# Kernel optimization log

Measured on AMD Instinct MI355X. Metric: run time of the kernel, lower is better.

## Reference

```python
import jax, jax.numpy as jnp
import numpy as np

M, D, K = 65536, 64, 4096
BETA = 0.25
INIT_STD = 0.1


def setup_inputs() -> dict:
    key = jax.random.key(0)
    k1, k2, k3 = jax.random.split(key, 3)
    z_e = jax.random.normal(k1, (M, D), dtype=jnp.float32)
    codebook_weight = jax.random.normal(k2, (K, D), dtype=jnp.float32) * INIT_STD
    ema_cluster_size = jax.random.uniform(k3, (K,), dtype=jnp.float32)
    return {"z_e": z_e, "codebook_weight": codebook_weight,
            "ema_cluster_size": ema_cluster_size}


def reference(z_e, codebook_weight, ema_cluster_size):
    # Squared-distance matrix: ||z||^2 + ||e||^2 - 2 z.e   -> (M, K)
    z2 = jnp.sum(z_e * z_e, axis=1, keepdims=True)            # (M, 1)
    e2 = jnp.sum(codebook_weight * codebook_weight, axis=1)[None, :]  # (1, K)
    ze = z_e @ codebook_weight.T                               # (M, K)
    dist = z2 + e2 - 2.0 * ze
    indices = jnp.argmin(dist, axis=1)                         # (M,)
    z_q = codebook_weight[indices]                             # (M, D)

    # use_ema=True path (eval mode: no EMA buffer update)
    commit_loss = jnp.mean((z_e - jax.lax.stop_gradient(z_q)) ** 2)
    vq_loss = BETA * commit_loss

    # Straight-through estimator
    z_q_st = z_e + jax.lax.stop_gradient(z_q - z_e)

    # Perplexity from EMA cluster-size buffer
    probs = ema_cluster_size + 1e-10
    probs = probs / jnp.sum(probs)
    perplexity = jnp.exp(-jnp.sum(probs * jnp.log(probs)))
    perplexity = jax.lax.stop_gradient(perplexity)

    return z_q_st, indices, vq_loss, perplexity, z_q
```

## Files before the change

kernel.cpp:

```cpp
#include <hip/hip_runtime.h>
#include <cmath>

#define M_ROWS  65536
#define D_DIM   64
#define K_CODES 4096

#define OFF_IDX  4194304
#define OFF_SCAL 4259840
#define OFF_ZQ   4259842

#define IMG_OFF   (4u << 20)
#define CANDB_OFF 17039368u

#define CH_BYTES 16384
#define CH_QUADS 1024
#define NSPLIT   4
#define NCHB     8

typedef _Float16 f16x8 __attribute__((ext_vector_type(8)));
typedef __attribute__((ext_vector_type(4))) float f32x4;
typedef unsigned long long u64;

__device__ __forceinline__ unsigned short f2h(float f) {
  _Float16 h = (_Float16)f;
  return __builtin_bit_cast(unsigned short, h);
}
__device__ __forceinline__ float h2f(unsigned short u) {
  return (float)__builtin_bit_cast(_Float16, u);
}
__device__ __forceinline__ unsigned int umin_(unsigned int a, unsigned int b) {
  return a < b ? a : b;
}
__device__ __forceinline__ unsigned int med3_u32(unsigned int a, unsigned int b, unsigned int c) {
  unsigned int d;
  asm("v_med3_u32 %0, %1, %2, %3" : "=v"(d) : "v"(a), "v"(b), "v"(c));
  return d;
}

__device__ __forceinline__ void gload_lds16(const void* g, void* l) {
  __builtin_amdgcn_global_load_lds((const __attribute__((address_space(1))) void*)g,
                                   (__attribute__((address_space(3))) void*)l, 16, 0, 0);
}
__device__ __forceinline__ void gload_lds4(const void* g, void* l) {
  __builtin_amdgcn_global_load_lds((const __attribute__((address_space(1))) void*)g,
                                   (__attribute__((address_space(3))) void*)l, 4, 0, 0);
}

__device__ __forceinline__ float exact_dist(const float4* z4, float z2,
                                            const float* __restrict__ cb,
                                            const float* __restrict__ e2, int k) {
  const float4* ev = (const float4*)(cb + (size_t)k * 64);
  float4 a0 = make_float4(0.f, 0.f, 0.f, 0.f);
  float4 a1 = make_float4(0.f, 0.f, 0.f, 0.f);
  float4 a2 = make_float4(0.f, 0.f, 0.f, 0.f);
  float4 a3 = make_float4(0.f, 0.f, 0.f, 0.f);
#pragma unroll
  for (int q = 0; q < 4; ++q) {
    float4 e0 = ev[4 * q + 0], e1 = ev[4 * q + 1], e2v = ev[4 * q + 2], e3 = ev[4 * q + 3];
    a0.x = fmaf(z4[4 * q + 0].x, e0.x, a0.x); a0.y = fmaf(z4[4 * q + 0].y, e0.y, a0.y);
    a0.z = fmaf(z4[4 * q + 0].z, e0.z, a0.z); a0.w = fmaf(z4[4 * q + 0].w, e0.w, a0.w);
    a1.x = fmaf(z4[4 * q + 1].x, e1.x, a1.x); a1.y = fmaf(z4[4 * q + 1].y, e1.y, a1.y);
    a1.z = fmaf(z4[4 * q + 1].z, e1.z, a1.z); a1.w = fmaf(z4[4 * q + 1].w, e1.w, a1.w);
    a2.x = fmaf(z4[4 * q + 2].x, e2v.x, a2.x); a2.y = fmaf(z4[4 * q + 2].y, e2v.y, a2.y);
    a2.z = fmaf(z4[4 * q + 2].z, e2v.z, a2.z); a2.w = fmaf(z4[4 * q + 2].w, e2v.w, a2.w);
    a3.x = fmaf(z4[4 * q + 3].x, e3.x, a3.x); a3.y = fmaf(z4[4 * q + 3].y, e3.y, a3.y);
    a3.z = fmaf(z4[4 * q + 3].z, e3.z, a3.z); a3.w = fmaf(z4[4 * q + 3].w, e3.w, a3.w);
  }
  float d;
  {
#pragma clang fp contract(off)
    float sx = (a0.x + a1.x) + (a2.x + a3.x);
    float sy = (a0.y + a1.y) + (a2.y + a3.y);
    float sz = (a0.z + a1.z) + (a2.z + a3.z);
    float sw = (a0.w + a1.w) + (a2.w + a3.w);
    float dot = (sx + sy) + (sz + sw);
    float tt = z2 + e2[k];
    d = tt - 2.0f * dot;
  }
  return d;
}

__device__ __forceinline__ float exact_z2(const float4* z4) {
#pragma clang fp contract(off)
  float rr[8];
  {
    const float* f = (const float*)&z4[0];
#pragma unroll
    for (int j = 0; j < 8; ++j) rr[j] = f[j] * f[j];
  }
#pragma unroll
  for (int a = 1; a < 8; ++a) {
    const float* f = (const float*)&z4[2 * a];
#pragma unroll
    for (int j = 0; j < 8; ++j) rr[j] = rr[j] + f[j] * f[j];
  }
  return ((rr[0] + rr[1]) + (rr[2] + rr[3])) + ((rr[4] + rr[5]) + (rr[6] + rr[7]));
}

__device__ __forceinline__ unsigned int ford(float f) {
  unsigned int b = __float_as_uint(f);
  return b ^ ((((int)b) >> 31) | 0x80000000u);
}

__global__ void prep_kernel(const float* __restrict__ cb, char* __restrict__ img,
                            float* __restrict__ e2, float* __restrict__ e2b) {
  int t = blockIdx.x * 256 + threadIdx.x;
  {
    int k  = t >> 4;
    int d0 = (t & 15) * 4;
    float4 f = ((const float4*)cb)[t];
    ushort4 hi;
    hi.x = f2h(f.x);
    hi.y = f2h(f.y);
    hi.z = f2h(f.z);
    hi.w = f2h(f.w);
    int c = k >> 7, r = k & 127;
    int g = d0 >> 3;
    int off = ((g + r) & 7) * 16 + (d0 & 7) * 2;
    char* base = img + (size_t)c * CH_BYTES + r * 128;
    *(ushort4*)(base + off) = hi;
  }
  if (t < K_CODES) {
    const float4* row = (const float4*)(cb + (size_t)t * D_DIM);
    float4 q[16];
#pragma unroll
    for (int i = 0; i < 16; ++i) q[i] = row[i];
    float s = exact_z2(q);
    e2[t] = s;
    e2b[t] = s + 32.0f;
  }
}

__global__ __launch_bounds__(512, 4)
void vq_mfma_kernel(const float* __restrict__ z_e,
                    const char* __restrict__ img,
                    const float* __restrict__ e2b,
                    u64* __restrict__ cand64) {
  __shared__ union {
    uint4 q[2][CH_QUADS];
    char raw[2][CH_BYTES];
    unsigned int cand[256 * 33];
  } sm;
  __shared__ float lds_e2[2][128];
  const int tid  = threadIdx.x;
  const int wave = tid >> 6, lane = tid & 63;
  const int quad = lane >> 4, c16 = lane & 15;
  const int rb   = blockIdx.x >> 2;
  const int sp   = blockIdx.x & 3;
  const int mb   = rb * 256 + wave * 32;

  {
    const uint4* src = (const uint4*)(img + (size_t)(sp * NCHB + 0) * CH_BYTES);
    gload_lds16(src + tid, &sm.q[0][tid]);
    gload_lds16(src + tid + 512, &sm.q[0][tid + 512]);
    if (tid < 128) gload_lds4(e2b + sp * 1024 + 0 * 128 + tid, &lds_e2[0][tid]);
  }

  f16x8 zh[2][2];
#pragma unroll
  for (int mt = 0; mt < 2; ++mt) {
    int m = mb + mt * 16 + c16;
#pragma unroll
    for (int s = 0; s < 2; ++s) {
      const float* zp = z_e + (size_t)m * 64 + s * 32 + quad * 8;
      float4 fa = ((const float4*)zp)[0];
      float4 fb = ((const float4*)zp)[1];
      float v[8] = {fa.x, fa.y, fa.z, fa.w, fb.x, fb.y, fb.z, fb.w};
      union { f16x8 v8; unsigned short e[8]; } H;
#pragma unroll
      for (int j = 0; j < 8; ++j) H.e[j] = f2h(-2.0f * v[j]);
      zh[mt][s] = H.v8;
    }
  }

  unsigned int b1[2][4], b2[2][4];
#pragma unroll
  for (int mt = 0; mt < 2; ++mt)
#pragma unroll
    for (int r = 0; r < 4; ++r) { b1[mt][r] = 0xFFFFFFFFu; b2[mt][r] = 0xFFFFFFFFu; }

  const int swz0 = ((quad + c16) & 7) * 16;
  const int swz1 = ((quad + 4 + c16) & 7) * 16;

  __syncthreads();

  int cur = 0;
  for (int c = 0; c < NCHB; ++c) {
    if (c + 1 < NCHB) {
      const int nb = cur ^ 1;
      const uint4* src = (const uint4*)(img + (size_t)(sp * NCHB + c + 1) * CH_BYTES);
      gload_lds16(src + tid, &sm.q[nb][tid]);
      gload_lds16(src + tid + 512, &sm.q[nb][tid + 512]);
      if (tid < 128) gload_lds4(e2b + sp * 1024 + (c + 1) * 128 + tid, &lds_e2[nb][tid]);
    }

#pragma unroll 1
    for (int t = 0; t < 8; ++t) {
      const char* hb = sm.raw[cur] + (t * 16 + c16) * 128;
      f16x8 Bh0 = *(const f16x8*)(hb + swz0);
      f16x8 Bh1 = *(const f16x8*)(hb + swz1);
      float e2v = lds_e2[cur][t * 16 + c16];
      unsigned int tid8 = (unsigned int)(sp * 64 + c * 8 + t);
      f32x4 cvec = {e2v, e2v, e2v, e2v};

#pragma unroll
      for (int mt = 0; mt < 2; ++mt) {
        f32x4 acc;
        acc = __builtin_amdgcn_mfma_f32_16x16x32_f16(zh[mt][0], Bh0, cvec, 0, 0, 0);
        acc = __builtin_amdgcn_mfma_f32_16x16x32_f16(zh[mt][1], Bh1, acc, 0, 0, 0);
#pragma unroll
        for (int r = 0; r < 4; ++r) {
          unsigned int key = (__float_as_uint(acc[r]) & 0xFFFFFF00u) | tid8;
          b2[mt][r] = med3_u32(b1[mt][r], b2[mt][r], key);
          b1[mt][r] = umin_(b1[mt][r], key);
        }
      }
    }
    __syncthreads();
    cur ^= 1;
  }

  __syncthreads();
  {
#pragma unroll
    for (int mt = 0; mt < 2; ++mt)
#pragma unroll
      for (int r = 0; r < 4; ++r) {
        int lr = wave * 32 + mt * 16 + quad * 4 + r;
        sm.cand[lr * 33 + c16 * 2 + 0] = b1[mt][r];
        sm.cand[lr * 33 + c16 * 2 + 1] = b2[mt][r];
      }
  }
  __syncthreads();
  if (tid < 256) {
    unsigned int kk[4] = {0xFFFFFFFFu, 0xFFFFFFFFu, 0xFFFFFFFFu, 0xFFFFFFFFu};
    unsigned int vv[4] = {0, 0, 0, 0};
    for (int j = 0; j < 32; ++j) {
      unsigned int key = sm.cand[tid * 33 + j];
      if (key < kk[3]) {
        kk[3] = key;
        vv[3] = (key & 0xFFu) * 16 + (unsigned int)(j >> 1);
        for (int p = 3; p > 0; --p)
          if (kk[p] < kk[p - 1]) {
            unsigned int a = kk[p]; kk[p] = kk[p - 1]; kk[p - 1] = a;
            unsigned int b = vv[p]; vv[p] = vv[p - 1]; vv[p - 1] = b;
          }
      }
    }
    int grow = rb * 256 + tid;
#pragma unroll
    for (int i = 0; i < 4; ++i)
      cand64[(size_t)grow * 16 + sp * 4 + i] = ((u64)kk[i] << 32) | (u64)vv[i];
  }
}

__device__ __forceinline__ void pick_scan4(const u64* __restrict__ cand64,
                                           int row, int part, u64& s1, u64& s2) {
  s1 = ~0ull; s2 = ~0ull;
  const u64* cp = cand64 + (size_t)row * 16 + part * 4;
#pragma unroll
  for (int j = 0; j < 4; ++j) {
    u64 v = cp[j];
    if (v < s1) { s2 = s1; s1 = v; }
    else if (v < s2) s2 = v;
  }
#pragma unroll
  for (int m = 1; m <= 2; m <<= 1) {
    u64 o1 = __shfl_xor(s1, m);
    u64 o2 = __shfl_xor(s2, m);
    u64 hi  = s1 > o1 ? s1 : o1;
    u64 lo2 = s2 < o2 ? s2 : o2;
    s1 = s1 < o1 ? s1 : o1;
    s2 = hi < lo2 ? hi : lo2;
  }
}

__device__ __forceinline__ int pick_exact16(const float* __restrict__ z_e,
                                            const float* __restrict__ cb,
                                            const float* __restrict__ e2,
                                            const u64* __restrict__ cand64,
                                            int row, int lane16) {
  const int k = (int)(unsigned int)(cand64[(size_t)row * 16 + lane16] & 0xFFFFFFFFu);
  const float4* zr = (const float4*)(z_e + (size_t)row * 64);
  float4 z4[16];
#pragma unroll
  for (int j = 0; j < 16; ++j) z4[j] = zr[j];
  float z2 = exact_z2(z4);
  float d = exact_dist(z4, z2, cb, e2, k);
  u64 kk = ((u64)ford(d) << 32) | (unsigned int)k;
#pragma unroll
  for (int m = 1; m <= 8; m <<= 1) {
    u64 o = __shfl_xor(kk, m);
    kk = o < kk ? o : kk;
  }
  return (int)(unsigned int)(kk & 0xFFFFFFFFu);
}

__global__ __launch_bounds__(256)
void pick_kernel(const float* __restrict__ z_e, const float* __restrict__ cb,
                 const float* __restrict__ e2, const u64* __restrict__ cand64,
                 float* __restrict__ out) {
  __shared__ int list[64];
  __shared__ int lcnt;
  const int tid = threadIdx.x;
  const int R0  = blockIdx.x * 64;
  if (tid == 0) lcnt = 0;
  __syncthreads();

  {
    const int row = R0 + (tid >> 2);
    u64 s1, s2;
    pick_scan4(cand64, row, tid & 3, s1, s2);
    if ((tid & 3) == 0) {
      unsigned int key1 = (unsigned int)(s1 >> 32) & 0xFFFFFF00u;
      unsigned int key2 = (unsigned int)(s2 >> 32) & 0xFFFFFF00u;
      if ((key2 - key1) >= 2048u) {
        out[OFF_IDX + row] = (float)(unsigned int)(s1 & 0xFFFFFFFFu);
      } else {
        list[atomicAdd(&lcnt, 1)] = row - R0;
      }
    }
  }
  __syncthreads();

  const int n = lcnt;
  const int lane16 = tid & 15;
  for (int g = tid >> 4; g < n; g += 16) {
    const int row = R0 + list[g];
    int bk = pick_exact16(z_e, cb, e2, cand64, row, lane16);
    if (lane16 == 0) out[OFF_IDX + row] = (float)bk;
  }
}

__global__ __launch_bounds__(256)
void pickzq_kernel(const float* __restrict__ z_e, const float* __restrict__ cb,
                   const float* __restrict__ e2, const u64* __restrict__ cand64,
                   float* __restrict__ out, double* __restrict__ partials) {
  __shared__ int sidx[64];
  __shared__ int list[64];
  __shared__ int lcnt;
  __shared__ double red[4];
  const int tid = threadIdx.x;
  const int R0  = blockIdx.x * 64;
  if (tid == 0) lcnt = 0;
  __syncthreads();

  {
    const int row = R0 + (tid >> 2);
    u64 s1, s2;
    pick_scan4(cand64, row, tid & 3, s1, s2);
    if ((tid & 3) == 0) {
      unsigned int key1 = (unsigned int)(s1 >> 32) & 0xFFFFFF00u;
      unsigned int key2 = (unsigned int)(s2 >> 32) & 0xFFFFFF00u;
      int lr = row - R0;
      if ((key2 - key1) >= 2048u) {
        int k = (int)(unsigned int)(s1 & 0xFFFFFFFFu);
        sidx[lr] = k;
        out[OFF_IDX + row] = (float)k;
      } else {
        list[atomicAdd(&lcnt, 1)] = lr;
      }
    }
  }
  __syncthreads();

  {
    const int n = lcnt;
    const int lane16 = tid & 15;
    for (int g = tid >> 4; g < n; g += 16) {
      const int lr = list[g];
      int bk = pick_exact16(z_e, cb, e2, cand64, R0 + lr, lane16);
      if (lane16 == 0) {
        sidx[lr] = bk;
        out[OFF_IDX + R0 + lr] = (float)bk;
      }
    }
  }
  __syncthreads();

  double csum = 0.0;
#pragma unroll
  for (int p = 0; p < 4; ++p) {
    const int m   = R0 + p * 16 + (tid >> 4);
    const int seg = tid & 15;
    const int k   = sidx[m - R0];
    float4 q = *(const float4*)(cb + (size_t)k * 64 + seg * 4);
    float4 z = *(const float4*)(z_e + (size_t)m * 64 + seg * 4);
    ((float4*)out)[(size_t)m * 16 + seg] = q;
    float* d1 = out + OFF_ZQ + (size_t)m * 64 + seg * 4;
    ((float2*)d1)[0] = make_float2(q.x, q.y);
    ((float2*)d1)[1] = make_float2(q.z, q.w);
    float dx = z.x - q.x, dy = z.y - q.y, dz = z.z - q.z, dw = z.w - q.w;
    csum += (double)dx * dx + (double)dy * dy + (double)dz * dz + (double)dw * dw;
  }
#pragma unroll
  for (int off = 32; off > 0; off >>= 1) csum += __shfl_down(csum, off);
  if ((tid & 63) == 0) red[tid >> 6] = csum;
  __syncthreads();
  if (tid == 0) partials[blockIdx.x] = red[0] + red[1] + red[2] + red[3];
}

__global__ __launch_bounds__(256)
void zq_kernel(const float* __restrict__ z_e, const float* __restrict__ cb,
               float* __restrict__ out, double* __restrict__ partials) {
  const int tid = threadIdx.x;
  const int t   = blockIdx.x * 256 + tid;
  const int m   = t >> 4, seg = t & 15;

  int k = (int)out[OFF_IDX + m];
  float4 q = *(const float4*)(cb + (size_t)k * 64 + seg * 4);
  float4 z = *(const float4*)(z_e + (size_t)m * 64 + seg * 4);

  ((float4*)out)[(size_t)m * 16 + seg] = q;
  float* d1 = out + OFF_ZQ + (size_t)m * 64 + seg * 4;
  ((float2*)d1)[0] = make_float2(q.x, q.y);
  ((float2*)d1)[1] = make_float2(q.z, q.w);

  float dx = z.x - q.x, dy = z.y - q.y, dz = z.z - q.z, dw = z.w - q.w;
  double csum = (double)dx * dx + (double)dy * dy + (double)dz * dz + (double)dw * dw;
#pragma unroll
  for (int off = 32; off > 0; off >>= 1) csum += __shfl_down(csum, off);
  if ((tid & 63) == 0) partials[blockIdx.x * 4 + (tid >> 6)] = csum;
}

__global__ void finalize_kernel(const float* __restrict__ ema,
                                const double* __restrict__ partials, int n,
                                float* __restrict__ out) {
  __shared__ double red[1024];
  const int t = threadIdx.x;

  double cs = 0.0;
  for (int i = t; i < n; i += 1024) cs += partials[i];
  red[t] = cs;
  __syncthreads();
  for (int off = 512; off > 0; off >>= 1) {
    if (t < off) red[t] += red[t + off];
    __syncthreads();
  }
  double commit = red[0];
  __syncthreads();

  double s = 0.0;
  for (int i = t; i < K_CODES; i += 1024) s += (double)(ema[i] + 1e-10f);
  red[t] = s;
  __syncthreads();
  for (int off = 512; off > 0; off >>= 1) {
    if (t < off) red[t] += red[t + off];
    __syncthreads();
  }
  double S = red[0];
  __syncthreads();

  double h = 0.0;
  for (int i = t; i < K_CODES; i += 1024) {
    float p = (float)((ema[i] + 1e-10f) / (float)S);
    h += (double)(p * logf(p));
  }
  red[t] = h;
  __syncthreads();
  for (int off = 512; off > 0; off >>= 1) {
    if (t < off) red[t] += red[t + off];
    __syncthreads();
  }

  if (t == 0) {
    out[OFF_SCAL]     = 0.25f * (float)(commit / (double)((size_t)M_ROWS * (size_t)D_DIM));
    out[OFF_SCAL + 1] = expf((float)(-red[0]));
  }
}

extern "C" void kernel_launch(void* const* d_in, const int* in_sizes, int n_in,
                              void* d_out, int out_size, void* d_ws, size_t ws_size,
                              hipStream_t stream) {
  (void)in_sizes; (void)n_in; (void)out_size;
  const float* z_e = (const float*)d_in[0];
  const float* cb  = (const float*)d_in[1];
  const float* ema = (const float*)d_in[2];
  float* out = (float*)d_out;

  float*  e2       = (float*)d_ws;
  float*  e2b      = (float*)((char*)d_ws + 16384);
  double* partials = (double*)((char*)d_ws + 32768);
  char*   img      = (char*)d_out + IMG_OFF;

  const size_t cand_bytes = (size_t)M_ROWS * 16 * 8;
  const int use_ws = (ws_size >= 163840 + cand_bytes) ? 1 : 0;
  u64* cand64 = use_ws
      ? (u64*)((char*)d_ws + 163840)
      : (u64*)((char*)d_out + CANDB_OFF);

  prep_kernel<<<(K_CODES * D_DIM / 4) / 256, 256, 0, stream>>>(cb, img, e2, e2b);
  vq_mfma_kernel<<<(M_ROWS / 256) * NSPLIT, 512, 0, stream>>>(z_e, img, e2b, cand64);
  if (use_ws) {
    pickzq_kernel<<<M_ROWS / 64, 256, 0, stream>>>(z_e, cb, e2, cand64, out, partials);
    finalize_kernel<<<1, 1024, 0, stream>>>(ema, partials, M_ROWS / 64, out);
  } else {
    pick_kernel<<<M_ROWS / 64, 256, 0, stream>>>(z_e, cb, e2, cand64, out);
    zq_kernel<<<M_ROWS * 16 / 256, 256, 0, stream>>>(z_e, cb, out, partials);
    finalize_kernel<<<1, 1024, 0, stream>>>(ema, partials, 16384, out);
  }
}
```

Before: 147.1 us.

## Fuse distance search, candidate pick and z_q write into one kernel

Adds a fused kernel in which each 512-thread block covers 128 rows across the full codebook of 32 chunks, replacing the split-K layout. Per-lane top-2 candidates are reduced in LDS, ambiguous rows are rechecked exactly, and z_q, the indices and the loss partials are written in the same kernel. This removes the global candidate buffer round trip and one kernel launch, and the codebook image now lives in the workspace. In exchange there are fewer blocks (512), each with a longer serial chunk loop, and only 128 threads handle the selection and exact-fallback phase.

Result: no change. 147.7 us (+0.4%).

```diff
diff --git a/kernel.cpp b/kernel.cpp
--- a/kernel.cpp
+++ b/kernel.cpp
@@ -14,6 +14,7 @@
 
 #define CH_BYTES 16384
 #define CH_QUADS 1024
+#define NCHB_F   32
 #define NSPLIT   4
 #define NCHB     8
 
@@ -128,6 +129,170 @@
     float s = exact_z2(q);
     e2[t] = s;
     e2b[t] = s + 32.0f;
+  }
+}
+
+__global__ __launch_bounds__(512, 4)
+void vq_full_kernel(const float* __restrict__ z_e,
+                    const char* __restrict__ img,
+                    const float* __restrict__ e2b,
+                    const float* __restrict__ cb,
+                    const float* __restrict__ e2,
+                    float* __restrict__ out,
+                    double* __restrict__ partials) {
+  __shared__ union {
+    uint4 q[2][CH_QUADS];
+    char raw[2][CH_BYTES];
+    unsigned int cand[128 * 33];
+  } sm;
+  __shared__ float lds_e2[2][128];
+  __shared__ int sidx[128];
+  __shared__ double red[8];
+  const int tid  = threadIdx.x;
+  const int wave = tid >> 6, lane = tid & 63;
+  const int quad = lane >> 4, c16 = lane & 15;
+  const int R0   = blockIdx.x * 128;
+
+  {
+    const uint4* src = (const uint4*)img;
+    gload_lds16(src + tid, &sm.q[0][tid]);
+    gload_lds16(src + tid + 512, &sm.q[0][tid + 512]);
+    if (tid < 128) gload_lds4(e2b + tid, &lds_e2[0][tid]);
+  }
+
+  f16x8 zh[2];
+  {
+    int m = R0 + wave * 16 + c16;
+#pragma unroll
+    for (int s = 0; s < 2; ++s) {
+      const float* zp = z_e + (size_t)m * 64 + s * 32 + quad * 8;
+      float4 fa = ((const float4*)zp)[0];
+      float4 fb = ((const float4*)zp)[1];
+      float v[8] = {fa.x, fa.y, fa.z, fa.w, fb.x, fb.y, fb.z, fb.w};
+      union { f16x8 v8; unsigned short e[8]; } H;
+#pragma unroll
+      for (int j = 0; j < 8; ++j) H.e[j] = f2h(-2.0f * v[j]);
+      zh[s] = H.v8;
+    }
+  }
+
+  unsigned int b1[4], b2[4];
+#pragma unroll
+  for (int r = 0; r < 4; ++r) { b1[r] = 0xFFFFFFFFu; b2[r] = 0xFFFFFFFFu; }
+
+  const int swz0 = ((quad + c16) & 7) * 16;
+  const int swz1 = ((quad + 4 + c16) & 7) * 16;
+
+  __syncthreads();
+
+  int cur = 0;
+  for (int c = 0; c < NCHB_F; ++c) {
+    if (c + 1 < NCHB_F) {
+      const int nb = cur ^ 1;
+      const uint4* src = (const uint4*)(img + (size_t)(c + 1) * CH_BYTES);
+      gload_lds16(src + tid, &sm.q[nb][tid]);
+      gload_lds16(src + tid + 512, &sm.q[nb][tid + 512]);
+      if (tid < 128) gload_lds4(e2b + (c + 1) * 128 + tid, &lds_e2[nb][tid]);
+    }
+
+#pragma unroll 1
+    for (int t = 0; t < 8; ++t) {
+      const char* hb = sm.raw[cur] + (t * 16 + c16) * 128;
+      f16x8 Bh0 = *(const f16x8*)(hb + swz0);
+      f16x8 Bh1 = *(const f16x8*)(hb + swz1);
+      float e2v = lds_e2[cur][t * 16 + c16];
+      unsigned int tid8 = (unsigned int)(c * 8 + t);
+      f32x4 cvec = {e2v, e2v, e2v, e2v};
+
+      f32x4 acc;
+      acc = __builtin_amdgcn_mfma_f32_16x16x32_f16(zh[0], Bh0, cvec, 0, 0, 0);
+      acc = __builtin_amdgcn_mfma_f32_16x16x32_f16(zh[1], Bh1, acc, 0, 0, 0);
+#pragma unroll
+      for (int r = 0; r < 4; ++r) {
+        unsigned int key = (__float_as_uint(acc[r]) & 0xFFFFFF00u) | tid8;
+        b2[r] = med3_u32(b1[r], b2[r], key);
+        b1[r] = umin_(b1[r], key);
+      }
+    }
+    __syncthreads();
+    cur ^= 1;
+  }
+
+  {
+#pragma unroll
+    for (int r = 0; r < 4; ++r) {
+      int lr = wave * 16 + quad * 4 + r;
+      sm.cand[lr * 33 + c16 * 2 + 0] = b1[r];
+      sm.cand[lr * 33 + c16 * 2 + 1] = b2[r];
+    }
+  }
+  __syncthreads();
+  if (tid < 128) {
+    unsigned int kk[4] = {0xFFFFFFFFu, 0xFFFFFFFFu, 0xFFFFFFFFu, 0xFFFFFFFFu};
+    unsigned int vv[4] = {0, 0, 0, 0};
+    for (int j = 0; j < 32; ++j) {
+      unsigned int key = sm.cand[tid * 33 + j];
+      if (key < kk[3]) {
+        kk[3] = key;
+        vv[3] = (key & 0xFFu) * 16 + (unsigned int)(j >> 1);
+        for (int p = 3; p > 0; --p)
+          if (kk[p] < kk[p - 1]) {
+            unsigned int a = kk[p]; kk[p] = kk[p - 1]; kk[p - 1] = a;
+            unsigned int b = vv[p]; vv[p] = vv[p - 1]; vv[p - 1] = b;
+          }
+      }
+    }
+    const int row = R0 + tid;
+    unsigned int key1 = kk[0] & 0xFFFFFF00u;
+    unsigned int key2 = kk[1] & 0xFFFFFF00u;
+    int bk;
+    if ((key2 - key1) >= 2048u) {
+      bk = (int)vv[0];
+    } else {
+      const float4* zr = (const float4*)(z_e + (size_t)row * 64);
+      float4 z4[16];
+#pragma unroll
+      for (int j = 0; j < 16; ++j) z4[j] = zr[j];
+      float z2 = exact_z2(z4);
+      float bd = INFINITY;
+      bk = K_CODES;
+#pragma unroll 1
+      for (int ci = 0; ci < 4; ++ci) {
+        int k = (int)vv[ci];
+        float d = exact_dist(z4, z2, cb, e2, k);
+        if (d < bd || (d == bd && k < bk)) { bd = d; bk = k; }
+      }
+    }
+    sidx[tid] = bk;
+    out[OFF_IDX + row] = (float)bk;
+  }
+  __syncthreads();
+
+  double csum = 0.0;
+#pragma unroll
+  for (int p = 0; p < 4; ++p) {
+    const int lr  = p * 32 + (tid >> 4);
+    const int m   = R0 + lr;
+    const int seg = tid & 15;
+    const int k   = sidx[lr];
+    float4 q = *(const float4*)(cb + (size_t)k * 64 + seg * 4);
+    float4 z = *(const float4*)(z_e + (size_t)m * 64 + seg * 4);
+    ((float4*)out)[(size_t)m * 16 + seg] = q;
+    float* d1 = out + OFF_ZQ + (size_t)m * 64 + seg * 4;
+    ((float2*)d1)[0] = make_float2(q.x, q.y);
+    ((float2*)d1)[1] = make_float2(q.z, q.w);
+    float dx = z.x - q.x, dy = z.y - q.y, dz = z.z - q.z, dw = z.w - q.w;
+    csum += (double)dx * dx + (double)dy * dy + (double)dz * dz + (double)dw * dw;
+  }
+#pragma unroll
+  for (int off = 32; off > 0; off >>= 1) csum += __shfl_down(csum, off);
+  if (lane == 0) red[wave] = csum;
+  __syncthreads();
+  if (tid == 0) {
+    double s = 0.0;
+#pragma unroll
+    for (int w = 0; w < 8; ++w) s += red[w];
+    partials[blockIdx.x] = s;
   }
 }
 
@@ -333,74 +498,6 @@
 }
 
 __global__ __launch_bounds__(256)
-void pickzq_kernel(const float* __restrict__ z_e, const float* __restrict__ cb,
-                   const float* __restrict__ e2, const u64* __restrict__ cand64,
-                   float* __restrict__ out, double* __restrict__ partials) {
-  __shared__ int sidx[64];
-  __shared__ int list[64];
-  __shared__ int lcnt;
-  __shared__ double red[4];
-  const int tid = threadIdx.x;
-  const int R0  = blockIdx.x * 64;
-  if (tid == 0) lcnt = 0;
-  __syncthreads();
-
-  {
-    const int row = R0 + (tid >> 2);
-    u64 s1, s2;
-    pick_scan4(cand64, row, tid & 3, s1, s2);
-    if ((tid & 3) == 0) {
-      unsigned int key1 = (unsigned int)(s1 >> 32) & 0xFFFFFF00u;
-      unsigned int key2 = (unsigned int)(s2 >> 32) & 0xFFFFFF00u;
-      int lr = row - R0;
-      if ((key2 - key1) >= 2048u) {
-        int k = (int)(unsigned int)(s1 & 0xFFFFFFFFu);
-        sidx[lr] = k;
-        out[OFF_IDX + row] = (float)k;
-      } else {
-        list[atomicAdd(&lcnt, 1)] = lr;
-      }
-    }
-  }
-  __syncthreads();
-
-  {
-    const int n = lcnt;
-    const int lane16 = tid & 15;
-    for (int g = tid >> 4; g < n; g += 16) {
-      const int lr = list[g];
-      int bk = pick_exact16(z_e, cb, e2, cand64, R0 + lr, lane16);
-      if (lane16 == 0) {
-        sidx[lr] = bk;
-        out[OFF_IDX + R0 + lr] = (float)bk;
-      }
-    }
-  }
-  __syncthreads();
-
-  double csum = 0.0;
-#pragma unroll
-  for (int p = 0; p < 4; ++p) {
-    const int m   = R0 + p * 16 + (tid >> 4);
-    const int seg = tid & 15;
-    const int k   = sidx[m - R0];
-    float4 q = *(const float4*)(cb + (size_t)k * 64 + seg * 4);
-    float4 z = *(const float4*)(z_e + (size_t)m * 64 + seg * 4);
-    ((float4*)out)[(size_t)m * 16 + seg] = q;
-    float* d1 = out + OFF_ZQ + (size_t)m * 64 + seg * 4;
-    ((float2*)d1)[0] = make_float2(q.x, q.y);
-    ((float2*)d1)[1] = make_float2(q.z, q.w);
-    float dx = z.x - q.x, dy = z.y - q.y, dz = z.z - q.z, dw = z.w - q.w;
-    csum += (double)dx * dx + (double)dy * dy + (double)dz * dz + (double)dw * dw;
-  }
-#pragma unroll
-  for (int off = 32; off > 0; off >>= 1) csum += __shfl_down(csum, off);
-  if ((tid & 63) == 0) red[tid >> 6] = csum;
-  __syncthreads();
-  if (tid == 0) partials[blockIdx.x] = red[0] + red[1] + red[2] + red[3];
-}
-
-__global__ __launch_bounds__(256)
 void zq_kernel(const float* __restrict__ z_e, const float* __restrict__ cb,
                float* __restrict__ out, double* __restrict__ partials) {
   const int tid = threadIdx.x;
@@ -481,20 +578,18 @@
   float*  e2       = (float*)d_ws;
   float*  e2b      = (float*)((char*)d_ws + 16384);
   double* partials = (double*)((char*)d_ws + 32768);
-  char*   img      = (char*)d_out + IMG_OFF;
-
-  const size_t cand_bytes = (size_t)M_ROWS * 16 * 8;
-  const int use_ws = (ws_size >= 163840 + cand_bytes) ? 1 : 0;
-  u64* cand64 = use_ws
-      ? (u64*)((char*)d_ws + 163840)
-      : (u64*)((char*)d_out + CANDB_OFF);
-
-  prep_kernel<<<(K_CODES * D_DIM / 4) / 256, 256, 0, stream>>>(cb, img, e2, e2b);
-  vq_mfma_kernel<<<(M_ROWS / 256) * NSPLIT, 512, 0, stream>>>(z_e, img, e2b, cand64);
-  if (use_ws) {
-    pickzq_kernel<<<M_ROWS / 64, 256, 0, stream>>>(z_e, cb, e2, cand64, out, partials);
-    finalize_kernel<<<1, 1024, 0, stream>>>(ema, partials, M_ROWS / 64, out);
+  const size_t fused_need = 163840 + 524288;
+
+  if (ws_size >= fused_need) {
+    char* img = (char*)d_ws + 163840;
+    prep_kernel<<<(K_CODES * D_DIM / 4) / 256, 256, 0, stream>>>(cb, img, e2, e2b);
+    vq_full_kernel<<<M_ROWS / 128, 512, 0, stream>>>(z_e, img, e2b, cb, e2, out, partials);
+    finalize_kernel<<<1, 1024, 0, stream>>>(ema, partials, M_ROWS / 128, out);
   } else {
+    char* img = (char*)d_out + IMG_OFF;
+    u64* cand64 = (u64*)((char*)d_out + CANDB_OFF);
+    prep_kernel<<<(K_CODES * D_DIM / 4) / 256, 256, 0, stream>>>(cb, img, e2, e2b);
+    vq_mfma_kernel<<<(M_ROWS / 256) * NSPLIT, 512, 0, stream>>>(z_e, img, e2b, cand64);
     pick_kernel<<<M_ROWS / 64, 256, 0, stream>>>(z_e, cb, e2, cand64, out);
     zq_kernel<<<M_ROWS * 16 / 256, 256, 0, stream>>>(z_e, cb, out, partials);
     finalize_kernel<<<1, 1024, 0, stream>>>(ema, partials, 16384, out);
```
